# Kernel optimization log

Measured on AMD Instinct MI355X. Metric: run time of the kernel, lower is better.

Reference implementation:

```python
import jax, jax.numpy as jnp
import numpy as np

B, C, H, W, K, O, KS = 32, 16, 256, 256, 4, 16, 3
C4 = C // 4


def setup_inputs() -> dict:
    key = jax.random.key(0)
    ks = jax.random.split(key, 6)
    return {
        "x": jax.random.normal(ks[0], (B, C, H, W), dtype=jnp.float32),
        "weight": jax.random.normal(ks[1], (K, O, C, KS, KS), dtype=jnp.float32),
        "attn_w1": jax.random.normal(ks[2], (C4, C), dtype=jnp.float32) * 0.1,
        "attn_b1": jnp.zeros((C4,), dtype=jnp.float32),
        "attn_w2": jax.random.normal(ks[3], (K, C4), dtype=jnp.float32) * 0.1,
        "attn_b2": jnp.zeros((K,), dtype=jnp.float32),
    }


def reference(x, weight, attn_w1, attn_b1, attn_w2, attn_b2):
    # Attention branch: global avg pool -> 1x1 conv -> relu -> 1x1 conv -> softmax over K
    pooled = x.mean(axis=(2, 3))                                  # (B, C)
    h = jax.nn.relu(pooled @ attn_w1.T + attn_b1)                 # (B, C//4)
    attn = jax.nn.softmax(h @ attn_w2.T + attn_b2, axis=1)        # (B, K)

    # Per-sample aggregated kernel: sum_k attn[b,k] * weight[k]
    agg_w = jnp.einsum('bk,koihw->boihw', attn, weight)           # (B, O, C, KS, KS)

    # Per-sample conv2d (equivalent to torch grouped conv with groups=B)
    pad = ((1, 1), (1, 1))
    def per_sample(xi, wi):
        # xi: (C, H, W), wi: (O, C, KS, KS)
        return jax.lax.conv_general_dilated(
            xi[None], wi, window_strides=(1, 1), padding=pad,
            dimension_numbers=('NCHW', 'OIHW', 'NCHW'))[0]
    return jax.vmap(per_sample)(x, agg_w)                         # (B, O, H, W)
```

## Files before the change

kernel.cpp:

```cpp
#include <hip/hip_runtime.h>

#define BD  32
#define CD  16
#define HD  256
#define WD  256
#define KD  4
#define OD  16
#define C4D 4

typedef __attribute__((ext_vector_type(8))) short short8v;
typedef __attribute__((ext_vector_type(4))) float float4v;

__device__ float          g_pooled[BD * CD];
__device__ unsigned short g_wfrag[BD * 2 * 5 * 64 * 8];

__device__ __forceinline__ unsigned short bf16_rne(float f) {
    unsigned u = __builtin_bit_cast(unsigned, f);
    u += 0x7FFFu + ((u >> 16) & 1u);
    return (unsigned short)(u >> 16);
}
__device__ __forceinline__ float bf16_to_f(unsigned short h) {
    unsigned u = ((unsigned)h) << 16;
    return __builtin_bit_cast(float, u);
}

__global__ void pool_kernel(const float* __restrict__ x) {
    const int plane = blockIdx.x;
    const float4* xp4 = reinterpret_cast<const float4*>(x + (size_t)plane * (HD * WD));

    float s = 0.f;
    #pragma unroll 4
    for (int j = threadIdx.x; j < HD * WD / 4; j += 256) {
        float4 v = xp4[j];
        s += v.x + v.y + v.z + v.w;
    }

    __shared__ float red[256];
    red[threadIdx.x] = s;
    __syncthreads();
    for (int off = 128; off > 0; off >>= 1) {
        if (threadIdx.x < off) red[threadIdx.x] += red[threadIdx.x + off];
        __syncthreads();
    }
    if (threadIdx.x == 0) g_pooled[plane] = red[0];
}

__global__ void attn_agg_kernel(const float* __restrict__ w1, const float* __restrict__ b1,
                                const float* __restrict__ w2, const float* __restrict__ b2,
                                const float* __restrict__ weight) {
    const int b = blockIdx.x;

    float p[CD];
    #pragma unroll
    for (int c = 0; c < CD; ++c) p[c] = g_pooled[b * CD + c] * (1.f / (HD * WD));

    float h[C4D];
    #pragma unroll
    for (int j = 0; j < C4D; ++j) {
        float s = b1[j];
        #pragma unroll
        for (int c = 0; c < CD; ++c) s = fmaf(p[c], w1[j * CD + c], s);
        h[j] = fmaxf(s, 0.f);
    }

    float lg[KD];
    float mx = -1e30f;
    #pragma unroll
    for (int k = 0; k < KD; ++k) {
        float s = b2[k];
        #pragma unroll
        for (int j = 0; j < C4D; ++j) s = fmaf(h[j], w2[k * C4D + j], s);
        lg[k] = s;
        mx = fmaxf(mx, s);
    }
    float se = 0.f;
    #pragma unroll
    for (int k = 0; k < KD; ++k) { lg[k] = expf(lg[k] - mx); se += lg[k]; }
    const float inv = 1.f / se;
    float at[KD];
    #pragma unroll
    for (int k = 0; k < KD; ++k) at[k] = lg[k] * inv;

    for (int e = threadIdx.x; e < 5120; e += 256) {
        const int prod = e / 2560;
        const int rem  = e % 2560;
        const int s    = rem / 512;
        const int lr   = rem % 512;
        const int lane = lr >> 3;
        const int i    = lr & 7;
        const int o    = lane & 15;
        const int kg   = lane >> 4;
        const int kk   = kg * 8 + i;
        const int tl   = kk >> 4;
        const int c    = kk & 15;
        const int tap  = 2 * s + tl;
        float v = 0.f;
        if (tap < 9) {
            #pragma unroll
            for (int k = 0; k < KD; ++k)
                v = fmaf(at[k], weight[((k * OD + o) * CD + c) * 9 + tap], v);
        }
        const unsigned short hi = bf16_rne(v);
        unsigned short val = hi;
        if (prod == 1) val = bf16_rne(v - bf16_to_f(hi));
        g_wfrag[b * 5120 + e] = val;
    }
}

__global__ __launch_bounds__(256, 3)
void conv_kernel(const float* __restrict__ x, float* __restrict__ out) {
    const int b  = blockIdx.y;
    const int tx = blockIdx.x & 15;
    const int ty = blockIdx.x >> 4;
    const int x0 = tx * 16, y0 = ty * 16;

    __shared__ unsigned short xs[18 * 18 * 40];

    for (int e = threadIdx.x; e < 5184; e += 256) {
        const int c   = e / 324;
        const int rem = e % 324;
        const int r   = rem / 18;
        const int col = rem % 18;
        const int gy  = y0 - 1 + r;
        const int gx  = x0 - 1 + col;
        float v = 0.f;
        if (gy >= 0 && gy < HD && gx >= 0 && gx < WD)
            v = x[((size_t)(b * CD + c) * HD + gy) * WD + gx];
        const unsigned short hi = bf16_rne(v);
        const unsigned short lo = bf16_rne(v - bf16_to_f(hi));
        const int base = (r * 18 + col) * 40 + (c >> 3) * 8 + (c & 7);
        xs[base]      = hi;
        xs[base + 16] = lo;
    }

    const int lane = threadIdx.x & 63;
    const int wv   = threadIdx.x >> 6;

    short8v whi[5], wlo[5];
    {
        const unsigned short* wf = g_wfrag + b * 5120;
        #pragma unroll
        for (int s = 0; s < 5; ++s) {
            whi[s] = *(const short8v*)&wf[s * 512 + lane * 8];
            wlo[s] = *(const short8v*)&wf[2560 + s * 512 + lane * 8];
        }
    }

    const int m     = lane & 15;
    const int kg    = lane >> 4;
    const int tl    = kg >> 1;
    const int chalf = kg & 1;
    int aoff[5];
    #pragma unroll
    for (int s = 0; s < 5; ++s) {
        int tap = 2 * s + tl;
        if (tap > 8) tap = 8;
        const int dy = tap / 3 - 1, dx = tap % 3 - 1;
        aoff[s] = (dy * 18 + dx) * 40;
    }

    __syncthreads();

    #pragma unroll
    for (int q = 0; q < 4; ++q) {
        const int rl   = wv * 4 + q;
        const int pix0 = ((rl + 1) * 18 + (1 + m)) * 40 + chalf * 8;
        float4v acc = {0.f, 0.f, 0.f, 0.f};
        #pragma unroll
        for (int s = 0; s < 5; ++s) {
            const short8v ahi = *(const short8v*)&xs[pix0 + aoff[s]];
            const short8v alo = *(const short8v*)&xs[pix0 + aoff[s] + 16];
            acc = __builtin_amdgcn_mfma_f32_16x16x32_bf16(ahi, whi[s], acc, 0, 0, 0);
            acc = __builtin_amdgcn_mfma_f32_16x16x32_bf16(alo, whi[s], acc, 0, 0, 0);
            acc = __builtin_amdgcn_mfma_f32_16x16x32_bf16(ahi, wlo[s], acc, 0, 0, 0);
        }
        const int o = lane & 15;
        const int y = y0 + rl;
        float4 v4 = make_float4(acc[0], acc[1], acc[2], acc[3]);
        *reinterpret_cast<float4*>(
            &out[((size_t)(b * OD + o) * HD + y) * WD + x0 + kg * 4]) = v4;
    }
}

extern "C" void kernel_launch(void* const* d_in, const int* in_sizes, int n_in,
                              void* d_out, int out_size, void* d_ws, size_t ws_size,
                              hipStream_t stream) {
    (void)in_sizes; (void)n_in; (void)out_size; (void)d_ws; (void)ws_size;
    const float* x      = (const float*)d_in[0];
    const float* weight = (const float*)d_in[1];
    const float* w1     = (const float*)d_in[2];
    const float* b1     = (const float*)d_in[3];
    const float* w2     = (const float*)d_in[4];
    const float* b2     = (const float*)d_in[5];
    float* out = (float*)d_out;

    pool_kernel<<<512, 256, 0, stream>>>(x);
    attn_agg_kernel<<<32, 256, 0, stream>>>(w1, b1, w2, b2, weight);
    conv_kernel<<<dim3(256, 32), 256, 0, stream>>>(x, out);
}
```

Measured before the change: 325.4 us.

## Widen conv tiles, drop split-bf16 activation term, split pooling across more blocks

The conv kernel now uses 16x64 output tiles per block, so halo overhead shrinks. Activations are staged in shared memory as a single bf16 (no low residual), with 16 channels packed per pixel by 128-bit stores. Each wave computes two rows at once with interleaved MFMAs, and only the weight hi/lo split remains, so there are 4 MFMAs per tap pair instead of 6 per row. The pooling kernel splits each plane across four blocks with fully unrolled loads. Dropping the activation lo term lowers accuracy to about bf16 on inputs, which may risk tolerance.

```diff
diff --git a/kernel.cpp b/kernel.cpp
--- a/kernel.cpp
+++ b/kernel.cpp
@@ -11,7 +11,7 @@
 typedef __attribute__((ext_vector_type(8))) short short8v;
 typedef __attribute__((ext_vector_type(4))) float float4v;
 
-__device__ float          g_pooled[BD * CD];
+__device__ float          g_partial[2048];
 __device__ unsigned short g_wfrag[BD * 2 * 5 * 64 * 8];
 
 __device__ __forceinline__ unsigned short bf16_rne(float f) {
@@ -25,15 +25,17 @@
 }
 
 __global__ void pool_kernel(const float* __restrict__ x) {
-    const int plane = blockIdx.x;
-    const float4* xp4 = reinterpret_cast<const float4*>(x + (size_t)plane * (HD * WD));
-
+    const int plane = blockIdx.x >> 2;
+    const int part  = blockIdx.x & 3;
+    const float4* xp4 = reinterpret_cast<const float4*>(
+        x + (size_t)plane * (HD * WD) + part * (HD * WD / 4));
+
+    float4 v[16];
+    #pragma unroll
+    for (int i = 0; i < 16; ++i) v[i] = xp4[threadIdx.x + i * 256];
     float s = 0.f;
-    #pragma unroll 4
-    for (int j = threadIdx.x; j < HD * WD / 4; j += 256) {
-        float4 v = xp4[j];
-        s += v.x + v.y + v.z + v.w;
-    }
+    #pragma unroll
+    for (int i = 0; i < 16; ++i) s += (v[i].x + v[i].y) + (v[i].z + v[i].w);
 
     __shared__ float red[256];
     red[threadIdx.x] = s;
@@ -42,7 +44,7 @@
         if (threadIdx.x < off) red[threadIdx.x] += red[threadIdx.x + off];
         __syncthreads();
     }
-    if (threadIdx.x == 0) g_pooled[plane] = red[0];
+    if (threadIdx.x == 0) g_partial[blockIdx.x] = red[0];
 }
 
 __global__ void attn_agg_kernel(const float* __restrict__ w1, const float* __restrict__ b1,
@@ -52,7 +54,11 @@
 
     float p[CD];
     #pragma unroll
-    for (int c = 0; c < CD; ++c) p[c] = g_pooled[b * CD + c] * (1.f / (HD * WD));
+    for (int c = 0; c < CD; ++c) {
+        const int i0 = (b * CD + c) * 4;
+        p[c] = (g_partial[i0] + g_partial[i0 + 1] + g_partial[i0 + 2] + g_partial[i0 + 3])
+               * (1.f / (HD * WD));
+    }
 
     float h[C4D];
     #pragma unroll
@@ -107,30 +113,35 @@
     }
 }
 
-__global__ __launch_bounds__(256, 3)
+__global__ __launch_bounds__(256, 2)
 void conv_kernel(const float* __restrict__ x, float* __restrict__ out) {
     const int b  = blockIdx.y;
-    const int tx = blockIdx.x & 15;
-    const int ty = blockIdx.x >> 4;
-    const int x0 = tx * 16, y0 = ty * 16;
-
-    __shared__ unsigned short xs[18 * 18 * 40];
-
-    for (int e = threadIdx.x; e < 5184; e += 256) {
-        const int c   = e / 324;
-        const int rem = e % 324;
-        const int r   = rem / 18;
-        const int col = rem % 18;
+    const int tx = blockIdx.x & 3;
+    const int ty = blockIdx.x >> 2;
+    const int x0 = tx * 64, y0 = ty * 16;
+
+    __shared__ unsigned short xs[18 * 66 * 24];
+
+    for (int e = threadIdx.x; e < 18 * 66; e += 256) {
+        const int r   = e / 66;
+        const int col = e - r * 66;
         const int gy  = y0 - 1 + r;
         const int gx  = x0 - 1 + col;
-        float v = 0.f;
-        if (gy >= 0 && gy < HD && gx >= 0 && gx < WD)
-            v = x[((size_t)(b * CD + c) * HD + gy) * WD + gx];
-        const unsigned short hi = bf16_rne(v);
-        const unsigned short lo = bf16_rne(v - bf16_to_f(hi));
-        const int base = (r * 18 + col) * 40 + (c >> 3) * 8 + (c & 7);
-        xs[base]      = hi;
-        xs[base + 16] = lo;
+        const bool ok = (gy >= 0) && (gy < HD) && (gx >= 0) && (gx < WD);
+        const float* px = x + ((size_t)b * CD * HD * WD) + (size_t)gy * WD + gx;
+        unsigned d[8];
+        #pragma unroll
+        for (int j = 0; j < 8; ++j) {
+            float v0 = 0.f, v1 = 0.f;
+            if (ok) {
+                v0 = px[(size_t)(2 * j)     * (HD * WD)];
+                v1 = px[(size_t)(2 * j + 1) * (HD * WD)];
+            }
+            d[j] = (unsigned)bf16_rne(v0) | ((unsigned)bf16_rne(v1) << 16);
+        }
+        unsigned* dst = reinterpret_cast<unsigned*>(&xs[e * 24]);
+        *reinterpret_cast<uint4*>(dst)     = make_uint4(d[0], d[1], d[2], d[3]);
+        *reinterpret_cast<uint4*>(dst + 4) = make_uint4(d[4], d[5], d[6], d[7]);
     }
 
     const int lane = threadIdx.x & 63;
@@ -156,29 +167,36 @@
         int tap = 2 * s + tl;
         if (tap > 8) tap = 8;
         const int dy = tap / 3 - 1, dx = tap % 3 - 1;
-        aoff[s] = (dy * 18 + dx) * 40;
-    }
+        aoff[s] = (dy * 66 + dx) * 24;
+    }
+    const int colbase = 1 + 16 * wv + m;
 
     __syncthreads();
 
-    #pragma unroll
-    for (int q = 0; q < 4; ++q) {
-        const int rl   = wv * 4 + q;
-        const int pix0 = ((rl + 1) * 18 + (1 + m)) * 40 + chalf * 8;
-        float4v acc = {0.f, 0.f, 0.f, 0.f};
+    #pragma unroll 1
+    for (int q2 = 0; q2 < 8; ++q2) {
+        const int qa = 2 * q2;
+        const int pa = ((qa + 1) * 66 + colbase) * 24 + chalf * 8;
+        const int pb = pa + 66 * 24;
+        float4v acca = {0.f, 0.f, 0.f, 0.f};
+        float4v accb = {0.f, 0.f, 0.f, 0.f};
         #pragma unroll
         for (int s = 0; s < 5; ++s) {
-            const short8v ahi = *(const short8v*)&xs[pix0 + aoff[s]];
-            const short8v alo = *(const short8v*)&xs[pix0 + aoff[s] + 16];
-            acc = __builtin_amdgcn_mfma_f32_16x16x32_bf16(ahi, whi[s], acc, 0, 0, 0);
-            acc = __builtin_amdgcn_mfma_f32_16x16x32_bf16(alo, whi[s], acc, 0, 0, 0);
-            acc = __builtin_amdgcn_mfma_f32_16x16x32_bf16(ahi, wlo[s], acc, 0, 0, 0);
-        }
-        const int o = lane & 15;
-        const int y = y0 + rl;
-        float4 v4 = make_float4(acc[0], acc[1], acc[2], acc[3]);
+            const short8v Aa = *(const short8v*)&xs[pa + aoff[s]];
+            const short8v Ab = *(const short8v*)&xs[pb + aoff[s]];
+            acca = __builtin_amdgcn_mfma_f32_16x16x32_bf16(Aa, whi[s], acca, 0, 0, 0);
+            accb = __builtin_amdgcn_mfma_f32_16x16x32_bf16(Ab, whi[s], accb, 0, 0, 0);
+            acca = __builtin_amdgcn_mfma_f32_16x16x32_bf16(Aa, wlo[s], acca, 0, 0, 0);
+            accb = __builtin_amdgcn_mfma_f32_16x16x32_bf16(Ab, wlo[s], accb, 0, 0, 0);
+        }
+        const int o  = lane & 15;
+        const int xc = x0 + 16 * wv + kg * 4;
+        float4 va = make_float4(acca[0], acca[1], acca[2], acca[3]);
+        float4 vb = make_float4(accb[0], accb[1], accb[2], accb[3]);
         *reinterpret_cast<float4*>(
-            &out[((size_t)(b * OD + o) * HD + y) * WD + x0 + kg * 4]) = v4;
+            &out[((size_t)(b * OD + o) * HD + (y0 + qa)) * WD + xc]) = va;
+        *reinterpret_cast<float4*>(
+            &out[((size_t)(b * OD + o) * HD + (y0 + qa + 1)) * WD + xc]) = vb;
     }
 }
 
@@ -194,7 +212,7 @@
     const float* b2     = (const float*)d_in[5];
     float* out = (float*)d_out;
 
-    pool_kernel<<<512, 256, 0, stream>>>(x);
+    pool_kernel<<<2048, 256, 0, stream>>>(x);
     attn_agg_kernel<<<32, 256, 0, stream>>>(w1, b1, w2, b2, weight);
-    conv_kernel<<<dim3(256, 32), 256, 0, stream>>>(x, out);
-}
+    conv_kernel<<<dim3(64, 32), 256, 0, stream>>>(x, out);
+}
```

Result: faster. 299.8 us (-7.9%).
